# Optimization experiments

Hardware: AMD Instinct MI355X
Metric: run time of the kernel (lower is better)

Reference implementation:

```python
import jax, jax.numpy as jnp
import numpy as np

B, N, D, K = 16, 65536, 24, 512
ATTRACTION_WEIGHT = 1.0
REPULSION_WEIGHT = 1.5
MARGIN_WEIGHT = 5.0
THRESHOLD = 0.5
MARGIN = 0.2
TAU = 0.7


def setup_inputs() -> dict:
    key = jax.random.key(0)
    k1, k2, k3 = jax.random.split(key, 3)
    beta = jax.random.normal(k1, (B, N, 1), jnp.float32)
    embed = jax.random.normal(k2, (B, N, D), jnp.float32)
    # First K hits of each event are the condensation points (one per instance),
    # remaining hits get a random instance id in [0, K).
    rand_sid = jax.random.randint(k3, (B, N - K), 0, K, jnp.int32)
    cp_sid = jnp.broadcast_to(jnp.arange(K, dtype=jnp.int32), (B, K))
    slice_id = jnp.concatenate([cp_sid, rand_sid], axis=1)
    is_cp = jnp.concatenate(
        [jnp.ones((B, K), jnp.int32), jnp.zeros((B, N - K), jnp.int32)], axis=1)
    return {"beta": beta, "embed": embed, "slice_id": slice_id, "is_cp": is_cp}


def _per_batch(beta_b, emb_b, sid, cp):
    # beta_b: [N], emb_b: [N, D], sid: [N] int, cp: [N] int
    n = beta_b.shape[0]
    f32 = beta_b.dtype
    cp_mask = cp == 1
    pos_count = cp_mask.sum()
    neg_count = n - pos_count

    seg_cnt = jax.ops.segment_sum(jnp.ones((n,), f32), sid, num_segments=K)
    inst_present = seg_cnt > 0
    cp_per_inst = jax.ops.segment_sum(cp_mask.astype(f32), sid, num_segments=K)
    valid_inst = inst_present & (cp_per_inst == 1)  # inst_cp.sum() == 1

    # --- grouped softmax CE over each instance (temperature TAU) ---
    logits = jnp.clip(beta_b, -20.0, 20.0) / TAU
    seg_max = jax.ops.segment_max(logits, sid, num_segments=K)
    safe_max = jnp.where(inst_present, seg_max, 0.0)
    ex = jnp.exp(logits - safe_max[sid])
    denom = jax.ops.segment_sum(ex, sid, num_segments=K)
    cp_logit = jax.ops.segment_sum(jnp.where(cp_mask, logits, 0.0), sid,
                                   num_segments=K)  # exactly one cp when valid
    p_cp = jnp.exp(cp_logit - safe_max) / jnp.maximum(denom, 1e-30)
    loss_inst = -jnp.log(p_cp + 1e-9)
    slice_count = valid_inst.sum()
    beta_slice_ce = jnp.where(valid_inst, loss_inst, 0.0).sum() / jnp.maximum(slice_count, 1)

    # --- margin loss on sigmoid(beta) ---
    beta_prob = jax.nn.sigmoid(jnp.clip(beta_b, -20.0, 20.0))
    pos_m = jnp.where(cp_mask, jax.nn.relu(THRESHOLD + MARGIN - beta_prob), 0.0).sum() \
        / jnp.maximum(pos_count, 1)
    neg_m = jnp.where(cp_mask, 0.0, jax.nn.relu(beta_prob - (THRESHOLD - MARGIN))).sum() \
        / jnp.maximum(neg_count, 1)
    beta_loss = beta_slice_ce + MARGIN_WEIGHT * (pos_m + neg_m)

    # --- attraction: hits pulled to first CP of their instance ---
    idx = jnp.arange(n, dtype=jnp.int32)
    first_cp = jax.ops.segment_min(jnp.where(cp_mask, idx, n), sid, num_segments=K)
    has_cp = (first_cp < n) & inst_present
    cp_emb = emb_b[jnp.minimum(first_cp, n - 1)]  # [K, D]
    d2 = jnp.minimum(((emb_b - cp_emb[sid]) ** 2).sum(-1), 50.0)
    d2_mean = jax.ops.segment_sum(d2, sid, num_segments=K) / jnp.maximum(seg_cnt, 1.0)
    attraction = ATTRACTION_WEIGHT * jnp.where(has_cp, d2_mean, 0.0).sum()

    # --- repulsion: pairwise exp(-d2) between CP embeddings (incl. diagonal) ---
    m = has_cp.astype(f32)
    mcount = m.sum()
    sq = (cp_emb ** 2).sum(-1)
    pd2 = sq[:, None] + sq[None, :] - 2.0 * (cp_emb @ cp_emb.T)
    pd2 = jnp.clip(pd2, 0.0, 50.0)
    rep = (jnp.exp(-pd2) * (m[:, None] * m[None, :])).sum() / jnp.maximum(mcount * mcount, 1.0)
    repulsion = jnp.where(mcount > 1, REPULSION_WEIGHT * rep, 0.0)

    valid = (pos_count >= 1) & (neg_count >= 1) & (slice_count > 0)
    total = beta_loss + attraction + repulsion
    return total, beta_loss, attraction, repulsion, valid


def reference(beta, embed, slice_id, is_cp):
    beta = jnp.nan_to_num(jnp.squeeze(beta, -1), nan=0.0, posinf=0.0, neginf=0.0)
    embed = jnp.nan_to_num(embed, nan=0.0, posinf=0.0, neginf=0.0)
    total, bl, al, rl, valid = jax.vmap(_per_batch)(beta, embed, slice_id, is_cp)
    v = valid.astype(beta.dtype)
    count = v.sum()
    safe = jnp.maximum(count, 1.0)
    ok = count > 0
    final = jnp.where(ok, (total * v).sum() / safe, 0.0)
    beta_log = jnp.where(ok, (bl * v).sum() / safe, 0.0)
    attr_log = jnp.where(ok, (al * v).sum() / safe, 0.0)
    repl_log = jnp.where(ok, (rl * v).sum() / safe, 0.0)
    return final, beta_log, attr_log, repl_log
```

## Files before the change

kernel.cpp:

```cpp
#include <hip/hip_runtime.h>
#include <math.h>

#define BB 16
#define NN 65536
#define DD 24
#define KK 512
#define CH 64
#define HPB (NN / CH)
#define TPB 256
#define RPB 8

__device__ __forceinline__ float fixnum(float v) {
  return __builtin_isfinite(v) ? v : 0.0f;
}

__device__ __forceinline__ float blockReduceSum(float v, float* sbuf) {
  __syncthreads();
  #pragma unroll
  for (int off = 32; off > 0; off >>= 1) v += __shfl_down(v, off, 64);
  int wid = threadIdx.x >> 6, lane = threadIdx.x & 63;
  if (lane == 0) sbuf[wid] = v;
  __syncthreads();
  return sbuf[0] + sbuf[1] + sbuf[2] + sbuf[3];
}

__global__ __launch_bounds__(TPB) void k1_seg(
    const float* __restrict__ beta, const int* __restrict__ sid,
    const int* __restrict__ iscp,
    float* __restrict__ cnt_p, float* __restrict__ den_p,
    float* __restrict__ cpc_p, float* __restrict__ cpl_p,
    int* __restrict__ first_p, float* __restrict__ marg_p)
{
  __shared__ float s_cnt[KK], s_den[KK], s_cpc[KK], s_cpl[KK];
  __shared__ int   s_first[KK];
  __shared__ float sred[4];
  int b = blockIdx.x >> 6, c = blockIdx.x & 63, t = threadIdx.x;
  for (int k = t; k < KK; k += TPB) {
    s_cnt[k] = 0.f; s_den[k] = 0.f; s_cpc[k] = 0.f; s_cpl[k] = 0.f; s_first[k] = NN;
  }
  __syncthreads();
  int h0 = c * HPB + t * 4;
  size_t g0 = (size_t)b * NN + h0;
  float4 bv = *(const float4*)(beta + g0);
  int4   sv = *(const int4*)(sid + g0);
  int4   cv = *(const int4*)(iscp + g0);
  float pm = 0.f, nm = 0.f;
  float bs[4] = {bv.x, bv.y, bv.z, bv.w};
  int   ss[4] = {sv.x, sv.y, sv.z, sv.w};
  int   cs[4] = {cv.x, cv.y, cv.z, cv.w};
  #pragma unroll
  for (int j = 0; j < 4; ++j) {
    float bc = fminf(fmaxf(fixnum(bs[j]), -20.f), 20.f);
    float logit = bc * (1.0f / 0.7f);
    int s = ss[j];
    atomicAdd(&s_cnt[s], 1.0f);
    atomicAdd(&s_den[s], __expf(logit));
    float prob = 1.0f / (1.0f + __expf(-bc));
    if (cs[j] == 1) {
      atomicAdd(&s_cpc[s], 1.0f);
      atomicAdd(&s_cpl[s], logit);
      atomicMin(&s_first[s], h0 + j);
      pm += fmaxf(0.7f - prob, 0.f);
    } else {
      nm += fmaxf(prob - 0.3f, 0.f);
    }
  }
  float pms = blockReduceSum(pm, sred);
  float nms = blockReduceSum(nm, sred);
  if (t == 0) { marg_p[2 * blockIdx.x] = pms; marg_p[2 * blockIdx.x + 1] = nms; }
  __syncthreads();
  size_t base = ((size_t)b * CH + c) * KK;
  for (int k = t; k < KK; k += TPB) {
    cnt_p[base + k] = s_cnt[k]; den_p[base + k] = s_den[k];
    cpc_p[base + k] = s_cpc[k]; cpl_p[base + k] = s_cpl[k];
    first_p[base + k] = s_first[k];
  }
}

__global__ __launch_bounds__(TPB) void k2_fin(
    const float* __restrict__ embed,
    const float* __restrict__ cnt_p, const float* __restrict__ den_p,
    const float* __restrict__ cpc_p, const float* __restrict__ cpl_p,
    const int* __restrict__ first_p,
    float* __restrict__ seg_cnt, float* __restrict__ loss_v,
    float* __restrict__ valid_f, float* __restrict__ has_cp_f,
    float* __restrict__ cpc_tot, float* __restrict__ cp_emb,
    float* __restrict__ d2_acc, float* __restrict__ rep_acc)
{
  int idx = blockIdx.x * TPB + threadIdx.x;
  int b = idx >> 9, k = idx & (KK - 1);
  float cnt = 0.f, den = 0.f, cpc = 0.f, cpl = 0.f;
  int fc = NN;
  #pragma unroll 8
  for (int c = 0; c < CH; ++c) {
    size_t base = ((size_t)b * CH + c) * KK + k;
    cnt += cnt_p[base]; den += den_p[base];
    cpc += cpc_p[base]; cpl += cpl_p[base];
    fc = min(fc, first_p[base]);
  }
  bool present = cnt > 0.f;
  bool vinst = present && (cpc == 1.0f);
  float p = __expf(cpl) / fmaxf(den, 1e-30f);
  seg_cnt[idx] = cnt;
  cpc_tot[idx] = cpc;
  loss_v[idx] = vinst ? -__logf(p + 1e-9f) : 0.f;
  valid_f[idx] = vinst ? 1.f : 0.f;
  has_cp_f[idx] = ((fc < NN) && present) ? 1.f : 0.f;
  d2_acc[idx] = 0.f;
  if (idx < BB) rep_acc[idx] = 0.f;
  int row = fc < NN ? fc : NN - 1;
  const float4* src = (const float4*)(embed + ((size_t)b * NN + row) * DD);
  float4* dst = (float4*)(cp_emb + (size_t)idx * DD);
  #pragma unroll
  for (int q = 0; q < DD / 4; ++q) {
    float4 v = src[q];
    v.x = fixnum(v.x); v.y = fixnum(v.y); v.z = fixnum(v.z); v.w = fixnum(v.w);
    dst[q] = v;
  }
}

__global__ __launch_bounds__(TPB) void k3_attr_rep(
    const float* __restrict__ embed, const int* __restrict__ sid,
    const float* __restrict__ cp_emb, const float* __restrict__ has_cp_f,
    float* __restrict__ d2_acc, float* __restrict__ rep_acc)
{
  __shared__ float s_d2[KK];
  __shared__ float sred[4];
  int b = blockIdx.x >> 6, c = blockIdx.x & 63, t = threadIdx.x;
  for (int k = t; k < KK; k += TPB) s_d2[k] = 0.f;
  __syncthreads();
  const float* cebase = cp_emb + (size_t)b * KK * DD;
  #pragma unroll
  for (int i = 0; i < HPB / TPB; ++i) {
    int h = c * HPB + i * TPB + t;
    size_t g = (size_t)b * NN + h;
    int s = sid[g];
    const float4* e  = (const float4*)(embed + g * DD);
    const float4* ce = (const float4*)(cebase + (size_t)s * DD);
    float d2 = 0.f;
    #pragma unroll
    for (int q = 0; q < DD / 4; ++q) {
      float4 ev = e[q]; float4 cv = ce[q];
      float x;
      x = fixnum(ev.x) - cv.x; d2 += x * x;
      x = fixnum(ev.y) - cv.y; d2 += x * x;
      x = fixnum(ev.z) - cv.z; d2 += x * x;
      x = fixnum(ev.w) - cv.w; d2 += x * x;
    }
    atomicAdd(&s_d2[s], fminf(d2, 50.f));
  }
  __syncthreads();
  for (int k = t; k < KK; k += TPB)
    atomicAdd(&d2_acc[b * KK + k], s_d2[k]);

  int j0 = t, j1 = t + TPB;
  float cj0[DD], cj1[DD];
  const float4* cj0p = (const float4*)(cebase + (size_t)j0 * DD);
  const float4* cj1p = (const float4*)(cebase + (size_t)j1 * DD);
  #pragma unroll
  for (int q = 0; q < DD / 4; ++q) {
    float4 a = cj0p[q], bq = cj1p[q];
    cj0[q*4] = a.x; cj0[q*4+1] = a.y; cj0[q*4+2] = a.z; cj0[q*4+3] = a.w;
    cj1[q*4] = bq.x; cj1[q*4+1] = bq.y; cj1[q*4+2] = bq.z; cj1[q*4+3] = bq.w;
  }
  float m0 = has_cp_f[b * KK + j0], m1 = has_cp_f[b * KK + j1];
  float acc = 0.f;
  #pragma unroll
  for (int ri = 0; ri < RPB; ++ri) {
    int i = c * RPB + ri;
    float mi = has_cp_f[b * KK + i];
    float d20 = 0.f, d21 = 0.f;
    #pragma unroll
    for (int d = 0; d < DD; ++d) {
      float ci = cebase[i * DD + d];
      float x0 = ci - cj0[d]; d20 += x0 * x0;
      float x1 = ci - cj1[d]; d21 += x1 * x1;
    }
    acc += mi * (m0 * __expf(-fminf(d20, 50.f)) + m1 * __expf(-fminf(d21, 50.f)));
  }
  float tot = blockReduceSum(acc, sred);
  if (t == 0) atomicAdd(&rep_acc[b], tot);
}

__global__ __launch_bounds__(1024) void k4_final(
    const float* __restrict__ d2_acc, const float* __restrict__ seg_cnt,
    const float* __restrict__ loss_v, const float* __restrict__ valid_f,
    const float* __restrict__ cpc_tot, const float* __restrict__ has_cp_f,
    const float* __restrict__ marg_p, const float* __restrict__ rep_acc,
    float* __restrict__ out)
{
  __shared__ float s_b[BB][5];
  int w = threadIdx.x >> 6, l = threadIdx.x & 63;
  int b = w;
  float attr = 0.f, ce = 0.f, vcnt = 0.f, pcnt = 0.f, mcnt = 0.f;
  #pragma unroll
  for (int k = l; k < KK; k += 64) {
    int idx = b * KK + k;
    float hc = has_cp_f[idx];
    attr += hc * (d2_acc[idx] / fmaxf(seg_cnt[idx], 1.f));
    ce   += loss_v[idx];
    vcnt += valid_f[idx];
    pcnt += cpc_tot[idx];
    mcnt += hc;
  }
  float pm = marg_p[(b * CH + l) * 2];
  float nm = marg_p[(b * CH + l) * 2 + 1];
  #pragma unroll
  for (int off = 32; off > 0; off >>= 1) {
    attr += __shfl_down(attr, off, 64);
    ce   += __shfl_down(ce, off, 64);
    vcnt += __shfl_down(vcnt, off, 64);
    pcnt += __shfl_down(pcnt, off, 64);
    mcnt += __shfl_down(mcnt, off, 64);
    pm   += __shfl_down(pm, off, 64);
    nm   += __shfl_down(nm, off, 64);
  }
  if (l == 0) {
    float pos = pcnt, neg = (float)NN - pos;
    float slice_ce = ce / fmaxf(vcnt, 1.f);
    float beta_loss = slice_ce + 5.0f * (pm / fmaxf(pos, 1.f) + nm / fmaxf(neg, 1.f));
    float rep = rep_acc[b] / fmaxf(mcnt * mcnt, 1.f);
    float repulsion = (mcnt > 1.f) ? 1.5f * rep : 0.f;
    float v = (pos >= 1.f && neg >= 1.f && vcnt > 0.f) ? 1.f : 0.f;
    s_b[w][0] = (beta_loss + attr + repulsion) * v;
    s_b[w][1] = beta_loss * v;
    s_b[w][2] = attr * v;
    s_b[w][3] = repulsion * v;
    s_b[w][4] = v;
  }
  __syncthreads();
  if (threadIdx.x == 0) {
    float s0 = 0.f, s1 = 0.f, s2 = 0.f, s3 = 0.f, cv = 0.f;
    #pragma unroll
    for (int i = 0; i < BB; ++i) {
      s0 += s_b[i][0]; s1 += s_b[i][1]; s2 += s_b[i][2]; s3 += s_b[i][3]; cv += s_b[i][4];
    }
    float safe = fmaxf(cv, 1.f);
    bool ok = cv > 0.f;
    out[0] = ok ? s0 / safe : 0.f;
    out[1] = ok ? s1 / safe : 0.f;
    out[2] = ok ? s2 / safe : 0.f;
    out[3] = ok ? s3 / safe : 0.f;
  }
}

extern "C" void kernel_launch(void* const* d_in, const int* in_sizes, int n_in,
                              void* d_out, int out_size, void* d_ws, size_t ws_size,
                              hipStream_t stream) {
  (void)in_sizes; (void)n_in; (void)out_size; (void)ws_size;
  const float* beta  = (const float*)d_in[0];
  const float* embed = (const float*)d_in[1];
  const int*   sid   = (const int*)d_in[2];
  const int*   iscp  = (const int*)d_in[3];
  float* out = (float*)d_out;
  char* ws = (char*)d_ws;

  size_t off = 0;
  auto alloc = [&](size_t bytes) {
    size_t o = off; off += (bytes + 255) & ~(size_t)255; return o;
  };
  const size_t BCK = (size_t)BB * CH * KK * 4;
  const size_t BKf = (size_t)BB * KK * 4;
  size_t o_cnt_p  = alloc(BCK);
  size_t o_den_p  = alloc(BCK);
  size_t o_cpc_p  = alloc(BCK);
  size_t o_cpl_p  = alloc(BCK);
  size_t o_first  = alloc(BCK);
  size_t o_marg   = alloc((size_t)BB * CH * 2 * 4);
  size_t o_segc   = alloc(BKf);
  size_t o_lossv  = alloc(BKf);
  size_t o_validf = alloc(BKf);
  size_t o_hascp  = alloc(BKf);
  size_t o_cpct   = alloc(BKf);
  size_t o_d2     = alloc(BKf);
  size_t o_cpe    = alloc((size_t)BB * KK * DD * 4);
  size_t o_rep    = alloc((size_t)BB * 4);

  k1_seg<<<BB * CH, TPB, 0, stream>>>(beta, sid, iscp,
      (float*)(ws + o_cnt_p), (float*)(ws + o_den_p),
      (float*)(ws + o_cpc_p), (float*)(ws + o_cpl_p),
      (int*)(ws + o_first), (float*)(ws + o_marg));

  k2_fin<<<(BB * KK) / TPB, TPB, 0, stream>>>(embed,
      (const float*)(ws + o_cnt_p), (const float*)(ws + o_den_p),
      (const float*)(ws + o_cpc_p), (const float*)(ws + o_cpl_p),
      (const int*)(ws + o_first),
      (float*)(ws + o_segc), (float*)(ws + o_lossv), (float*)(ws + o_validf),
      (float*)(ws + o_hascp), (float*)(ws + o_cpct), (float*)(ws + o_cpe),
      (float*)(ws + o_d2), (float*)(ws + o_rep));

  k3_attr_rep<<<BB * CH, TPB, 0, stream>>>(embed, sid,
      (const float*)(ws + o_cpe), (const float*)(ws + o_hascp),
      (float*)(ws + o_d2), (float*)(ws + o_rep));

  k4_final<<<1, 1024, 0, stream>>>((const float*)(ws + o_d2),
      (const float*)(ws + o_segc), (const float*)(ws + o_lossv),
      (const float*)(ws + o_validf), (const float*)(ws + o_cpct),
      (const float*)(ws + o_hascp), (const float*)(ws + o_marg),
      (const float*)(ws + o_rep), out);
}
```

Before: 200.3 us.

## Fuse four kernels into one cooperative kernel with grid syncs

Replaces the four-kernel pipeline with a single cooperative kernel that runs the segment pass, the finalisation, the attraction/repulsion pass and the final reduction as phases separated by grid.sync(). The chunk count per event is halved to 32, so the grid is 512 blocks (each k1-phase thread handles 8 hits and each block does 16 repulsion rows), and the finalisation phase uses 16-lane shuffle reductions. The aim is to remove kernel launch gaps and tail effects, at the cost of grid-wide barriers, reduced parallelism in the embed-heavy phase, and the requirement that all blocks be co-resident.

```diff
diff --git a/kernel.cpp b/kernel.cpp
--- a/kernel.cpp
+++ b/kernel.cpp
@@ -1,14 +1,17 @@
 #include <hip/hip_runtime.h>
+#include <hip/hip_cooperative_groups.h>
 #include <math.h>
+
+namespace cg = cooperative_groups;
 
 #define BB 16
 #define NN 65536
 #define DD 24
 #define KK 512
-#define CH 64
+#define CH 32
 #define HPB (NN / CH)
 #define TPB 256
-#define RPB 8
+#define RPB 16
 
 __device__ __forceinline__ float fixnum(float v) {
   return __builtin_isfinite(v) ? v : 0.0f;
@@ -24,223 +27,229 @@
   return sbuf[0] + sbuf[1] + sbuf[2] + sbuf[3];
 }
 
-__global__ __launch_bounds__(TPB) void k1_seg(
+__global__ __launch_bounds__(TPB, 2) void fused_all(
     const float* __restrict__ beta, const int* __restrict__ sid,
-    const int* __restrict__ iscp,
+    const int* __restrict__ iscp, const float* __restrict__ embed,
     float* __restrict__ cnt_p, float* __restrict__ den_p,
     float* __restrict__ cpc_p, float* __restrict__ cpl_p,
-    int* __restrict__ first_p, float* __restrict__ marg_p)
-{
-  __shared__ float s_cnt[KK], s_den[KK], s_cpc[KK], s_cpl[KK];
-  __shared__ int   s_first[KK];
-  __shared__ float sred[4];
-  int b = blockIdx.x >> 6, c = blockIdx.x & 63, t = threadIdx.x;
-  for (int k = t; k < KK; k += TPB) {
-    s_cnt[k] = 0.f; s_den[k] = 0.f; s_cpc[k] = 0.f; s_cpl[k] = 0.f; s_first[k] = NN;
-  }
-  __syncthreads();
-  int h0 = c * HPB + t * 4;
-  size_t g0 = (size_t)b * NN + h0;
-  float4 bv = *(const float4*)(beta + g0);
-  int4   sv = *(const int4*)(sid + g0);
-  int4   cv = *(const int4*)(iscp + g0);
-  float pm = 0.f, nm = 0.f;
-  float bs[4] = {bv.x, bv.y, bv.z, bv.w};
-  int   ss[4] = {sv.x, sv.y, sv.z, sv.w};
-  int   cs[4] = {cv.x, cv.y, cv.z, cv.w};
-  #pragma unroll
-  for (int j = 0; j < 4; ++j) {
-    float bc = fminf(fmaxf(fixnum(bs[j]), -20.f), 20.f);
-    float logit = bc * (1.0f / 0.7f);
-    int s = ss[j];
-    atomicAdd(&s_cnt[s], 1.0f);
-    atomicAdd(&s_den[s], __expf(logit));
-    float prob = 1.0f / (1.0f + __expf(-bc));
-    if (cs[j] == 1) {
-      atomicAdd(&s_cpc[s], 1.0f);
-      atomicAdd(&s_cpl[s], logit);
-      atomicMin(&s_first[s], h0 + j);
-      pm += fmaxf(0.7f - prob, 0.f);
-    } else {
-      nm += fmaxf(prob - 0.3f, 0.f);
-    }
-  }
-  float pms = blockReduceSum(pm, sred);
-  float nms = blockReduceSum(nm, sred);
-  if (t == 0) { marg_p[2 * blockIdx.x] = pms; marg_p[2 * blockIdx.x + 1] = nms; }
-  __syncthreads();
-  size_t base = ((size_t)b * CH + c) * KK;
-  for (int k = t; k < KK; k += TPB) {
-    cnt_p[base + k] = s_cnt[k]; den_p[base + k] = s_den[k];
-    cpc_p[base + k] = s_cpc[k]; cpl_p[base + k] = s_cpl[k];
-    first_p[base + k] = s_first[k];
-  }
-}
-
-__global__ __launch_bounds__(TPB) void k2_fin(
-    const float* __restrict__ embed,
-    const float* __restrict__ cnt_p, const float* __restrict__ den_p,
-    const float* __restrict__ cpc_p, const float* __restrict__ cpl_p,
-    const int* __restrict__ first_p,
+    int* __restrict__ first_p, float* __restrict__ marg_p,
     float* __restrict__ seg_cnt, float* __restrict__ loss_v,
     float* __restrict__ valid_f, float* __restrict__ has_cp_f,
     float* __restrict__ cpc_tot, float* __restrict__ cp_emb,
-    float* __restrict__ d2_acc, float* __restrict__ rep_acc)
+    float* __restrict__ d2_acc, float* __restrict__ rep_acc,
+    float* __restrict__ out)
 {
-  int idx = blockIdx.x * TPB + threadIdx.x;
-  int b = idx >> 9, k = idx & (KK - 1);
-  float cnt = 0.f, den = 0.f, cpc = 0.f, cpl = 0.f;
-  int fc = NN;
-  #pragma unroll 8
-  for (int c = 0; c < CH; ++c) {
-    size_t base = ((size_t)b * CH + c) * KK + k;
-    cnt += cnt_p[base]; den += den_p[base];
-    cpc += cpc_p[base]; cpl += cpl_p[base];
-    fc = min(fc, first_p[base]);
-  }
-  bool present = cnt > 0.f;
-  bool vinst = present && (cpc == 1.0f);
-  float p = __expf(cpl) / fmaxf(den, 1e-30f);
-  seg_cnt[idx] = cnt;
-  cpc_tot[idx] = cpc;
-  loss_v[idx] = vinst ? -__logf(p + 1e-9f) : 0.f;
-  valid_f[idx] = vinst ? 1.f : 0.f;
-  has_cp_f[idx] = ((fc < NN) && present) ? 1.f : 0.f;
-  d2_acc[idx] = 0.f;
-  if (idx < BB) rep_acc[idx] = 0.f;
-  int row = fc < NN ? fc : NN - 1;
-  const float4* src = (const float4*)(embed + ((size_t)b * NN + row) * DD);
-  float4* dst = (float4*)(cp_emb + (size_t)idx * DD);
-  #pragma unroll
-  for (int q = 0; q < DD / 4; ++q) {
-    float4 v = src[q];
-    v.x = fixnum(v.x); v.y = fixnum(v.y); v.z = fixnum(v.z); v.w = fixnum(v.w);
-    dst[q] = v;
-  }
-}
-
-__global__ __launch_bounds__(TPB) void k3_attr_rep(
-    const float* __restrict__ embed, const int* __restrict__ sid,
-    const float* __restrict__ cp_emb, const float* __restrict__ has_cp_f,
-    float* __restrict__ d2_acc, float* __restrict__ rep_acc)
-{
+  cg::grid_group grid = cg::this_grid();
+  __shared__ float s_cnt[KK], s_den[KK], s_cpc[KK], s_cpl[KK];
+  __shared__ int   s_first[KK];
   __shared__ float s_d2[KK];
   __shared__ float sred[4];
-  int b = blockIdx.x >> 6, c = blockIdx.x & 63, t = threadIdx.x;
-  for (int k = t; k < KK; k += TPB) s_d2[k] = 0.f;
+  __shared__ float s_b[BB][5];
+
+  int b = blockIdx.x / CH, c = blockIdx.x % CH, t = threadIdx.x;
+
+  for (int k = t; k < KK; k += TPB) {
+    s_cnt[k] = 0.f; s_den[k] = 0.f; s_cpc[k] = 0.f; s_cpl[k] = 0.f; s_first[k] = NN;
+  }
   __syncthreads();
-  const float* cebase = cp_emb + (size_t)b * KK * DD;
-  #pragma unroll
-  for (int i = 0; i < HPB / TPB; ++i) {
-    int h = c * HPB + i * TPB + t;
-    size_t g = (size_t)b * NN + h;
-    int s = sid[g];
-    const float4* e  = (const float4*)(embed + g * DD);
-    const float4* ce = (const float4*)(cebase + (size_t)s * DD);
-    float d2 = 0.f;
+  {
+    int h0 = c * HPB + t * 8;
+    size_t g0 = (size_t)b * NN + h0;
+    float pm = 0.f, nm = 0.f;
+    #pragma unroll
+    for (int half = 0; half < 2; ++half) {
+      size_t g = g0 + half * 4;
+      float4 bv = *(const float4*)(beta + g);
+      int4   sv = *(const int4*)(sid + g);
+      int4   cv = *(const int4*)(iscp + g);
+      float bs[4] = {bv.x, bv.y, bv.z, bv.w};
+      int   ss[4] = {sv.x, sv.y, sv.z, sv.w};
+      int   cs[4] = {cv.x, cv.y, cv.z, cv.w};
+      #pragma unroll
+      for (int j = 0; j < 4; ++j) {
+        float bc = fminf(fmaxf(fixnum(bs[j]), -20.f), 20.f);
+        float logit = bc * (1.0f / 0.7f);
+        int s = ss[j];
+        atomicAdd(&s_cnt[s], 1.0f);
+        atomicAdd(&s_den[s], __expf(logit));
+        float prob = 1.0f / (1.0f + __expf(-bc));
+        if (cs[j] == 1) {
+          atomicAdd(&s_cpc[s], 1.0f);
+          atomicAdd(&s_cpl[s], logit);
+          atomicMin(&s_first[s], h0 + half * 4 + j);
+          pm += fmaxf(0.7f - prob, 0.f);
+        } else {
+          nm += fmaxf(prob - 0.3f, 0.f);
+        }
+      }
+    }
+    float pms = blockReduceSum(pm, sred);
+    float nms = blockReduceSum(nm, sred);
+    if (t == 0) { marg_p[2 * blockIdx.x] = pms; marg_p[2 * blockIdx.x + 1] = nms; }
+    __syncthreads();
+    size_t base = ((size_t)b * CH + c) * KK;
+    for (int k = t; k < KK; k += TPB) {
+      cnt_p[base + k] = s_cnt[k]; den_p[base + k] = s_den[k];
+      cpc_p[base + k] = s_cpc[k]; cpl_p[base + k] = s_cpl[k];
+      first_p[base + k] = s_first[k];
+    }
+  }
+  grid.sync();
+
+  {
+    int sub = t >> 4, lane16 = t & 15;
+    int idx = blockIdx.x * 16 + sub;
+    int pb = idx >> 9, pk = idx & (KK - 1);
+    size_t base0 = ((size_t)pb * CH + lane16) * KK + pk;
+    size_t base1 = ((size_t)pb * CH + lane16 + 16) * KK + pk;
+    float cnt = cnt_p[base0] + cnt_p[base1];
+    float den = den_p[base0] + den_p[base1];
+    float cpc = cpc_p[base0] + cpc_p[base1];
+    float cpl = cpl_p[base0] + cpl_p[base1];
+    int fc = min(first_p[base0], first_p[base1]);
+    #pragma unroll
+    for (int m = 8; m > 0; m >>= 1) {
+      cnt += __shfl_xor(cnt, m, 16);
+      den += __shfl_xor(den, m, 16);
+      cpc += __shfl_xor(cpc, m, 16);
+      cpl += __shfl_xor(cpl, m, 16);
+      fc = min(fc, __shfl_xor(fc, m, 16));
+    }
+    if (lane16 == 0) {
+      bool present = cnt > 0.f;
+      bool vinst = present && (cpc == 1.0f);
+      float p = __expf(cpl) / fmaxf(den, 1e-30f);
+      seg_cnt[idx] = cnt;
+      cpc_tot[idx] = cpc;
+      loss_v[idx] = vinst ? -__logf(p + 1e-9f) : 0.f;
+      valid_f[idx] = vinst ? 1.f : 0.f;
+      has_cp_f[idx] = ((fc < NN) && present) ? 1.f : 0.f;
+      d2_acc[idx] = 0.f;
+      if (idx < BB) rep_acc[idx] = 0.f;
+    }
+    int row = fc < NN ? fc : NN - 1;
+    if (lane16 < DD / 4) {
+      const float4* src = (const float4*)(embed + ((size_t)pb * NN + row) * DD);
+      float4 v = src[lane16];
+      v.x = fixnum(v.x); v.y = fixnum(v.y); v.z = fixnum(v.z); v.w = fixnum(v.w);
+      ((float4*)(cp_emb + (size_t)idx * DD))[lane16] = v;
+    }
+  }
+  grid.sync();
+
+  {
+    for (int k = t; k < KK; k += TPB) s_d2[k] = 0.f;
+    __syncthreads();
+    const float* cebase = cp_emb + (size_t)b * KK * DD;
+    #pragma unroll
+    for (int i = 0; i < HPB / TPB; ++i) {
+      int h = c * HPB + i * TPB + t;
+      size_t g = (size_t)b * NN + h;
+      int s = sid[g];
+      const float4* e  = (const float4*)(embed + g * DD);
+      const float4* ce = (const float4*)(cebase + (size_t)s * DD);
+      float d2 = 0.f;
+      #pragma unroll
+      for (int q = 0; q < DD / 4; ++q) {
+        float4 ev = e[q]; float4 cv = ce[q];
+        float x;
+        x = fixnum(ev.x) - cv.x; d2 += x * x;
+        x = fixnum(ev.y) - cv.y; d2 += x * x;
+        x = fixnum(ev.z) - cv.z; d2 += x * x;
+        x = fixnum(ev.w) - cv.w; d2 += x * x;
+      }
+      atomicAdd(&s_d2[s], fminf(d2, 50.f));
+    }
+    __syncthreads();
+    for (int k = t; k < KK; k += TPB)
+      atomicAdd(&d2_acc[b * KK + k], s_d2[k]);
+
+    int j0 = t, j1 = t + TPB;
+    float cj0[DD], cj1[DD];
+    const float4* cj0p = (const float4*)(cebase + (size_t)j0 * DD);
+    const float4* cj1p = (const float4*)(cebase + (size_t)j1 * DD);
     #pragma unroll
     for (int q = 0; q < DD / 4; ++q) {
-      float4 ev = e[q]; float4 cv = ce[q];
-      float x;
-      x = fixnum(ev.x) - cv.x; d2 += x * x;
-      x = fixnum(ev.y) - cv.y; d2 += x * x;
-      x = fixnum(ev.z) - cv.z; d2 += x * x;
-      x = fixnum(ev.w) - cv.w; d2 += x * x;
-    }
-    atomicAdd(&s_d2[s], fminf(d2, 50.f));
-  }
-  __syncthreads();
-  for (int k = t; k < KK; k += TPB)
-    atomicAdd(&d2_acc[b * KK + k], s_d2[k]);
-
-  int j0 = t, j1 = t + TPB;
-  float cj0[DD], cj1[DD];
-  const float4* cj0p = (const float4*)(cebase + (size_t)j0 * DD);
-  const float4* cj1p = (const float4*)(cebase + (size_t)j1 * DD);
-  #pragma unroll
-  for (int q = 0; q < DD / 4; ++q) {
-    float4 a = cj0p[q], bq = cj1p[q];
-    cj0[q*4] = a.x; cj0[q*4+1] = a.y; cj0[q*4+2] = a.z; cj0[q*4+3] = a.w;
-    cj1[q*4] = bq.x; cj1[q*4+1] = bq.y; cj1[q*4+2] = bq.z; cj1[q*4+3] = bq.w;
-  }
-  float m0 = has_cp_f[b * KK + j0], m1 = has_cp_f[b * KK + j1];
-  float acc = 0.f;
-  #pragma unroll
-  for (int ri = 0; ri < RPB; ++ri) {
-    int i = c * RPB + ri;
-    float mi = has_cp_f[b * KK + i];
-    float d20 = 0.f, d21 = 0.f;
-    #pragma unroll
-    for (int d = 0; d < DD; ++d) {
-      float ci = cebase[i * DD + d];
-      float x0 = ci - cj0[d]; d20 += x0 * x0;
-      float x1 = ci - cj1[d]; d21 += x1 * x1;
-    }
-    acc += mi * (m0 * __expf(-fminf(d20, 50.f)) + m1 * __expf(-fminf(d21, 50.f)));
-  }
-  float tot = blockReduceSum(acc, sred);
-  if (t == 0) atomicAdd(&rep_acc[b], tot);
-}
-
-__global__ __launch_bounds__(1024) void k4_final(
-    const float* __restrict__ d2_acc, const float* __restrict__ seg_cnt,
-    const float* __restrict__ loss_v, const float* __restrict__ valid_f,
-    const float* __restrict__ cpc_tot, const float* __restrict__ has_cp_f,
-    const float* __restrict__ marg_p, const float* __restrict__ rep_acc,
-    float* __restrict__ out)
-{
-  __shared__ float s_b[BB][5];
-  int w = threadIdx.x >> 6, l = threadIdx.x & 63;
-  int b = w;
-  float attr = 0.f, ce = 0.f, vcnt = 0.f, pcnt = 0.f, mcnt = 0.f;
-  #pragma unroll
-  for (int k = l; k < KK; k += 64) {
-    int idx = b * KK + k;
-    float hc = has_cp_f[idx];
-    attr += hc * (d2_acc[idx] / fmaxf(seg_cnt[idx], 1.f));
-    ce   += loss_v[idx];
-    vcnt += valid_f[idx];
-    pcnt += cpc_tot[idx];
-    mcnt += hc;
-  }
-  float pm = marg_p[(b * CH + l) * 2];
-  float nm = marg_p[(b * CH + l) * 2 + 1];
-  #pragma unroll
-  for (int off = 32; off > 0; off >>= 1) {
-    attr += __shfl_down(attr, off, 64);
-    ce   += __shfl_down(ce, off, 64);
-    vcnt += __shfl_down(vcnt, off, 64);
-    pcnt += __shfl_down(pcnt, off, 64);
-    mcnt += __shfl_down(mcnt, off, 64);
-    pm   += __shfl_down(pm, off, 64);
-    nm   += __shfl_down(nm, off, 64);
-  }
-  if (l == 0) {
-    float pos = pcnt, neg = (float)NN - pos;
-    float slice_ce = ce / fmaxf(vcnt, 1.f);
-    float beta_loss = slice_ce + 5.0f * (pm / fmaxf(pos, 1.f) + nm / fmaxf(neg, 1.f));
-    float rep = rep_acc[b] / fmaxf(mcnt * mcnt, 1.f);
-    float repulsion = (mcnt > 1.f) ? 1.5f * rep : 0.f;
-    float v = (pos >= 1.f && neg >= 1.f && vcnt > 0.f) ? 1.f : 0.f;
-    s_b[w][0] = (beta_loss + attr + repulsion) * v;
-    s_b[w][1] = beta_loss * v;
-    s_b[w][2] = attr * v;
-    s_b[w][3] = repulsion * v;
-    s_b[w][4] = v;
-  }
-  __syncthreads();
-  if (threadIdx.x == 0) {
-    float s0 = 0.f, s1 = 0.f, s2 = 0.f, s3 = 0.f, cv = 0.f;
-    #pragma unroll
-    for (int i = 0; i < BB; ++i) {
-      s0 += s_b[i][0]; s1 += s_b[i][1]; s2 += s_b[i][2]; s3 += s_b[i][3]; cv += s_b[i][4];
-    }
-    float safe = fmaxf(cv, 1.f);
-    bool ok = cv > 0.f;
-    out[0] = ok ? s0 / safe : 0.f;
-    out[1] = ok ? s1 / safe : 0.f;
-    out[2] = ok ? s2 / safe : 0.f;
-    out[3] = ok ? s3 / safe : 0.f;
+      float4 a = cj0p[q], bq = cj1p[q];
+      cj0[q*4] = a.x; cj0[q*4+1] = a.y; cj0[q*4+2] = a.z; cj0[q*4+3] = a.w;
+      cj1[q*4] = bq.x; cj1[q*4+1] = bq.y; cj1[q*4+2] = bq.z; cj1[q*4+3] = bq.w;
+    }
+    float m0 = has_cp_f[b * KK + j0], m1 = has_cp_f[b * KK + j1];
+    float acc = 0.f;
+    #pragma unroll
+    for (int ri = 0; ri < RPB; ++ri) {
+      int i = c * RPB + ri;
+      float mi = has_cp_f[b * KK + i];
+      float d20 = 0.f, d21 = 0.f;
+      #pragma unroll
+      for (int d = 0; d < DD; ++d) {
+        float ci = cebase[i * DD + d];
+        float x0 = ci - cj0[d]; d20 += x0 * x0;
+        float x1 = ci - cj1[d]; d21 += x1 * x1;
+      }
+      acc += mi * (m0 * __expf(-fminf(d20, 50.f)) + m1 * __expf(-fminf(d21, 50.f)));
+    }
+    float tot = blockReduceSum(acc, sred);
+    if (t == 0) atomicAdd(&rep_acc[b], tot);
+  }
+  grid.sync();
+
+  if (blockIdx.x == 0) {
+    int w = t >> 6, l = t & 63;
+    #pragma unroll
+    for (int bb = 0; bb < 4; ++bb) {
+      int fb = w * 4 + bb;
+      float attr = 0.f, ce = 0.f, vcnt = 0.f, pcnt = 0.f, mcnt = 0.f;
+      #pragma unroll
+      for (int k = l; k < KK; k += 64) {
+        int idx = fb * KK + k;
+        float hc = has_cp_f[idx];
+        attr += hc * (d2_acc[idx] / fmaxf(seg_cnt[idx], 1.f));
+        ce   += loss_v[idx];
+        vcnt += valid_f[idx];
+        pcnt += cpc_tot[idx];
+        mcnt += hc;
+      }
+      float pm = (l < CH) ? marg_p[(fb * CH + l) * 2]     : 0.f;
+      float nm = (l < CH) ? marg_p[(fb * CH + l) * 2 + 1] : 0.f;
+      #pragma unroll
+      for (int off = 32; off > 0; off >>= 1) {
+        attr += __shfl_down(attr, off, 64);
+        ce   += __shfl_down(ce, off, 64);
+        vcnt += __shfl_down(vcnt, off, 64);
+        pcnt += __shfl_down(pcnt, off, 64);
+        mcnt += __shfl_down(mcnt, off, 64);
+        pm   += __shfl_down(pm, off, 64);
+        nm   += __shfl_down(nm, off, 64);
+      }
+      if (l == 0) {
+        float pos = pcnt, neg = (float)NN - pos;
+        float slice_ce = ce / fmaxf(vcnt, 1.f);
+        float beta_loss = slice_ce + 5.0f * (pm / fmaxf(pos, 1.f) + nm / fmaxf(neg, 1.f));
+        float rep = rep_acc[fb] / fmaxf(mcnt * mcnt, 1.f);
+        float repulsion = (mcnt > 1.f) ? 1.5f * rep : 0.f;
+        float v = (pos >= 1.f && neg >= 1.f && vcnt > 0.f) ? 1.f : 0.f;
+        s_b[fb][0] = (beta_loss + attr + repulsion) * v;
+        s_b[fb][1] = beta_loss * v;
+        s_b[fb][2] = attr * v;
+        s_b[fb][3] = repulsion * v;
+        s_b[fb][4] = v;
+      }
+    }
+    __syncthreads();
+    if (t == 0) {
+      float s0 = 0.f, s1 = 0.f, s2 = 0.f, s3 = 0.f, cv = 0.f;
+      #pragma unroll
+      for (int i = 0; i < BB; ++i) {
+        s0 += s_b[i][0]; s1 += s_b[i][1]; s2 += s_b[i][2]; s3 += s_b[i][3]; cv += s_b[i][4];
+      }
+      float safe = fmaxf(cv, 1.f);
+      bool ok = cv > 0.f;
+      out[0] = ok ? s0 / safe : 0.f;
+      out[1] = ok ? s1 / safe : 0.f;
+      out[2] = ok ? s2 / safe : 0.f;
+      out[3] = ok ? s3 / safe : 0.f;
+    }
   }
 }
 
@@ -276,26 +285,29 @@
   size_t o_cpe    = alloc((size_t)BB * KK * DD * 4);
   size_t o_rep    = alloc((size_t)BB * 4);
 
-  k1_seg<<<BB * CH, TPB, 0, stream>>>(beta, sid, iscp,
-      (float*)(ws + o_cnt_p), (float*)(ws + o_den_p),
-      (float*)(ws + o_cpc_p), (float*)(ws + o_cpl_p),
-      (int*)(ws + o_first), (float*)(ws + o_marg));
-
-  k2_fin<<<(BB * KK) / TPB, TPB, 0, stream>>>(embed,
-      (const float*)(ws + o_cnt_p), (const float*)(ws + o_den_p),
-      (const float*)(ws + o_cpc_p), (const float*)(ws + o_cpl_p),
-      (const int*)(ws + o_first),
-      (float*)(ws + o_segc), (float*)(ws + o_lossv), (float*)(ws + o_validf),
-      (float*)(ws + o_hascp), (float*)(ws + o_cpct), (float*)(ws + o_cpe),
-      (float*)(ws + o_d2), (float*)(ws + o_rep));
-
-  k3_attr_rep<<<BB * CH, TPB, 0, stream>>>(embed, sid,
-      (const float*)(ws + o_cpe), (const float*)(ws + o_hascp),
-      (float*)(ws + o_d2), (float*)(ws + o_rep));
-
-  k4_final<<<1, 1024, 0, stream>>>((const float*)(ws + o_d2),
-      (const float*)(ws + o_segc), (const float*)(ws + o_lossv),
-      (const float*)(ws + o_validf), (const float*)(ws + o_cpct),
-      (const float*)(ws + o_hascp), (const float*)(ws + o_marg),
-      (const float*)(ws + o_rep), out);
+  float* p_cnt  = (float*)(ws + o_cnt_p);
+  float* p_den  = (float*)(ws + o_den_p);
+  float* p_cpc  = (float*)(ws + o_cpc_p);
+  float* p_cpl  = (float*)(ws + o_cpl_p);
+  int*   p_fst  = (int*)(ws + o_first);
+  float* p_marg = (float*)(ws + o_marg);
+  float* p_segc = (float*)(ws + o_segc);
+  float* p_lv   = (float*)(ws + o_lossv);
+  float* p_vf   = (float*)(ws + o_validf);
+  float* p_hc   = (float*)(ws + o_hascp);
+  float* p_cpt  = (float*)(ws + o_cpct);
+  float* p_cpe  = (float*)(ws + o_cpe);
+  float* p_d2   = (float*)(ws + o_d2);
+  float* p_rep  = (float*)(ws + o_rep);
+
+  void* args[] = {
+    (void*)&beta, (void*)&sid, (void*)&iscp, (void*)&embed,
+    (void*)&p_cnt, (void*)&p_den, (void*)&p_cpc, (void*)&p_cpl,
+    (void*)&p_fst, (void*)&p_marg,
+    (void*)&p_segc, (void*)&p_lv, (void*)&p_vf, (void*)&p_hc,
+    (void*)&p_cpt, (void*)&p_cpe, (void*)&p_d2, (void*)&p_rep,
+    (void*)&out,
+  };
+  hipLaunchCooperativeKernel((const void*)fused_all, dim3(BB * CH), dim3(TPB),
+                             args, 0, stream);
 }
```

New measurement: 348.6 us. 74.0% more time.

## Fuse final reduction into attraction/repulsion kernel and halve k1 chunk count

Applied to the files above, without the earlier changes.

Folds the single-block final reduction into the attraction/repulsion kernel: the last block, found with an atomic done-counter and thread fences, reads the accumulators and writes the outputs, which removes one kernel launch. The segment-stats kernel now processes 8 hits per thread with 32 chunks per batch, halving the partial buffers that the finalize kernel must sum. The attraction loop is restructured to use a vectorized int4 sid load with 4 consecutive hits per thread. The cost is a serial tail where one block reduces all 16 batches, plus fewer blocks in k1 to fill the GPU.

```diff
diff --git a/kernel.cpp b/kernel.cpp
--- a/kernel.cpp
+++ b/kernel.cpp
@@ -5,8 +5,10 @@
 #define NN 65536
 #define DD 24
 #define KK 512
-#define CH 64
-#define HPB (NN / CH)
+#define CH1 32
+#define HPB1 (NN / CH1)
+#define CH3 64
+#define HPB3 (NN / CH3)
 #define TPB 256
 #define RPB 8
 
@@ -34,42 +36,46 @@
   __shared__ float s_cnt[KK], s_den[KK], s_cpc[KK], s_cpl[KK];
   __shared__ int   s_first[KK];
   __shared__ float sred[4];
-  int b = blockIdx.x >> 6, c = blockIdx.x & 63, t = threadIdx.x;
+  int b = blockIdx.x / CH1, c = blockIdx.x % CH1, t = threadIdx.x;
   for (int k = t; k < KK; k += TPB) {
     s_cnt[k] = 0.f; s_den[k] = 0.f; s_cpc[k] = 0.f; s_cpl[k] = 0.f; s_first[k] = NN;
   }
   __syncthreads();
-  int h0 = c * HPB + t * 4;
+  int h0 = c * HPB1 + t * 8;
   size_t g0 = (size_t)b * NN + h0;
-  float4 bv = *(const float4*)(beta + g0);
-  int4   sv = *(const int4*)(sid + g0);
-  int4   cv = *(const int4*)(iscp + g0);
   float pm = 0.f, nm = 0.f;
-  float bs[4] = {bv.x, bv.y, bv.z, bv.w};
-  int   ss[4] = {sv.x, sv.y, sv.z, sv.w};
-  int   cs[4] = {cv.x, cv.y, cv.z, cv.w};
   #pragma unroll
-  for (int j = 0; j < 4; ++j) {
-    float bc = fminf(fmaxf(fixnum(bs[j]), -20.f), 20.f);
-    float logit = bc * (1.0f / 0.7f);
-    int s = ss[j];
-    atomicAdd(&s_cnt[s], 1.0f);
-    atomicAdd(&s_den[s], __expf(logit));
-    float prob = 1.0f / (1.0f + __expf(-bc));
-    if (cs[j] == 1) {
-      atomicAdd(&s_cpc[s], 1.0f);
-      atomicAdd(&s_cpl[s], logit);
-      atomicMin(&s_first[s], h0 + j);
-      pm += fmaxf(0.7f - prob, 0.f);
-    } else {
-      nm += fmaxf(prob - 0.3f, 0.f);
+  for (int half = 0; half < 2; ++half) {
+    size_t g = g0 + half * 4;
+    float4 bv = *(const float4*)(beta + g);
+    int4   sv = *(const int4*)(sid + g);
+    int4   cv = *(const int4*)(iscp + g);
+    float bs[4] = {bv.x, bv.y, bv.z, bv.w};
+    int   ss[4] = {sv.x, sv.y, sv.z, sv.w};
+    int   cs[4] = {cv.x, cv.y, cv.z, cv.w};
+    #pragma unroll
+    for (int j = 0; j < 4; ++j) {
+      float bc = fminf(fmaxf(fixnum(bs[j]), -20.f), 20.f);
+      float logit = bc * (1.0f / 0.7f);
+      int s = ss[j];
+      atomicAdd(&s_cnt[s], 1.0f);
+      atomicAdd(&s_den[s], __expf(logit));
+      float prob = 1.0f / (1.0f + __expf(-bc));
+      if (cs[j] == 1) {
+        atomicAdd(&s_cpc[s], 1.0f);
+        atomicAdd(&s_cpl[s], logit);
+        atomicMin(&s_first[s], h0 + half * 4 + j);
+        pm += fmaxf(0.7f - prob, 0.f);
+      } else {
+        nm += fmaxf(prob - 0.3f, 0.f);
+      }
     }
   }
   float pms = blockReduceSum(pm, sred);
   float nms = blockReduceSum(nm, sred);
   if (t == 0) { marg_p[2 * blockIdx.x] = pms; marg_p[2 * blockIdx.x + 1] = nms; }
   __syncthreads();
-  size_t base = ((size_t)b * CH + c) * KK;
+  size_t base = ((size_t)b * CH1 + c) * KK;
   for (int k = t; k < KK; k += TPB) {
     cnt_p[base + k] = s_cnt[k]; den_p[base + k] = s_den[k];
     cpc_p[base + k] = s_cpc[k]; cpl_p[base + k] = s_cpl[k];
@@ -85,15 +91,16 @@
     float* __restrict__ seg_cnt, float* __restrict__ loss_v,
     float* __restrict__ valid_f, float* __restrict__ has_cp_f,
     float* __restrict__ cpc_tot, float* __restrict__ cp_emb,
-    float* __restrict__ d2_acc, float* __restrict__ rep_acc)
+    float* __restrict__ d2_acc, float* __restrict__ rep_acc,
+    unsigned* __restrict__ done)
 {
   int idx = blockIdx.x * TPB + threadIdx.x;
   int b = idx >> 9, k = idx & (KK - 1);
   float cnt = 0.f, den = 0.f, cpc = 0.f, cpl = 0.f;
   int fc = NN;
   #pragma unroll 8
-  for (int c = 0; c < CH; ++c) {
-    size_t base = ((size_t)b * CH + c) * KK + k;
+  for (int c = 0; c < CH1; ++c) {
+    size_t base = ((size_t)b * CH1 + c) * KK + k;
     cnt += cnt_p[base]; den += den_p[base];
     cpc += cpc_p[base]; cpl += cpl_p[base];
     fc = min(fc, first_p[base]);
@@ -108,6 +115,7 @@
   has_cp_f[idx] = ((fc < NN) && present) ? 1.f : 0.f;
   d2_acc[idx] = 0.f;
   if (idx < BB) rep_acc[idx] = 0.f;
+  if (idx == 0) *done = 0u;
   int row = fc < NN ? fc : NN - 1;
   const float4* src = (const float4*)(embed + ((size_t)b * NN + row) * DD);
   float4* dst = (float4*)(cp_emb + (size_t)idx * DD);
@@ -119,128 +127,147 @@
   }
 }
 
-__global__ __launch_bounds__(TPB) void k3_attr_rep(
+__global__ __launch_bounds__(TPB) void k3_attr_rep_fin(
     const float* __restrict__ embed, const int* __restrict__ sid,
     const float* __restrict__ cp_emb, const float* __restrict__ has_cp_f,
-    float* __restrict__ d2_acc, float* __restrict__ rep_acc)
+    const float* __restrict__ seg_cnt, const float* __restrict__ loss_v,
+    const float* __restrict__ valid_f, const float* __restrict__ cpc_tot,
+    const float* __restrict__ marg_p,
+    float* __restrict__ d2_acc, float* __restrict__ rep_acc,
+    unsigned* __restrict__ done, float* __restrict__ out)
 {
   __shared__ float s_d2[KK];
   __shared__ float sred[4];
-  int b = blockIdx.x >> 6, c = blockIdx.x & 63, t = threadIdx.x;
+  __shared__ float s_b[BB][5];
+  __shared__ int amLast;
+  int b = blockIdx.x / CH3, c = blockIdx.x % CH3, t = threadIdx.x;
   for (int k = t; k < KK; k += TPB) s_d2[k] = 0.f;
   __syncthreads();
   const float* cebase = cp_emb + (size_t)b * KK * DD;
-  #pragma unroll
-  for (int i = 0; i < HPB / TPB; ++i) {
-    int h = c * HPB + i * TPB + t;
-    size_t g = (size_t)b * NN + h;
-    int s = sid[g];
-    const float4* e  = (const float4*)(embed + g * DD);
-    const float4* ce = (const float4*)(cebase + (size_t)s * DD);
-    float d2 = 0.f;
-    #pragma unroll
-    for (int q = 0; q < DD / 4; ++q) {
-      float4 ev = e[q]; float4 cv = ce[q];
-      float x;
-      x = fixnum(ev.x) - cv.x; d2 += x * x;
-      x = fixnum(ev.y) - cv.y; d2 += x * x;
-      x = fixnum(ev.z) - cv.z; d2 += x * x;
-      x = fixnum(ev.w) - cv.w; d2 += x * x;
-    }
-    atomicAdd(&s_d2[s], fminf(d2, 50.f));
+  {
+    int h0 = c * HPB3 + t * 4;
+    size_t g0 = (size_t)b * NN + h0;
+    int4 sv = *(const int4*)(sid + g0);
+    int ss[4] = {sv.x, sv.y, sv.z, sv.w};
+    #pragma unroll
+    for (int j = 0; j < 4; ++j) {
+      const float4* e  = (const float4*)(embed + (g0 + j) * DD);
+      const float4* ce = (const float4*)(cebase + (size_t)ss[j] * DD);
+      float d2 = 0.f;
+      #pragma unroll
+      for (int q = 0; q < DD / 4; ++q) {
+        float4 ev = e[q]; float4 cv = ce[q];
+        float x;
+        x = fixnum(ev.x) - cv.x; d2 += x * x;
+        x = fixnum(ev.y) - cv.y; d2 += x * x;
+        x = fixnum(ev.z) - cv.z; d2 += x * x;
+        x = fixnum(ev.w) - cv.w; d2 += x * x;
+      }
+      atomicAdd(&s_d2[ss[j]], fminf(d2, 50.f));
+    }
   }
   __syncthreads();
   for (int k = t; k < KK; k += TPB)
     atomicAdd(&d2_acc[b * KK + k], s_d2[k]);
 
-  int j0 = t, j1 = t + TPB;
-  float cj0[DD], cj1[DD];
-  const float4* cj0p = (const float4*)(cebase + (size_t)j0 * DD);
-  const float4* cj1p = (const float4*)(cebase + (size_t)j1 * DD);
-  #pragma unroll
-  for (int q = 0; q < DD / 4; ++q) {
-    float4 a = cj0p[q], bq = cj1p[q];
-    cj0[q*4] = a.x; cj0[q*4+1] = a.y; cj0[q*4+2] = a.z; cj0[q*4+3] = a.w;
-    cj1[q*4] = bq.x; cj1[q*4+1] = bq.y; cj1[q*4+2] = bq.z; cj1[q*4+3] = bq.w;
-  }
-  float m0 = has_cp_f[b * KK + j0], m1 = has_cp_f[b * KK + j1];
-  float acc = 0.f;
-  #pragma unroll
-  for (int ri = 0; ri < RPB; ++ri) {
-    int i = c * RPB + ri;
-    float mi = has_cp_f[b * KK + i];
-    float d20 = 0.f, d21 = 0.f;
-    #pragma unroll
-    for (int d = 0; d < DD; ++d) {
-      float ci = cebase[i * DD + d];
-      float x0 = ci - cj0[d]; d20 += x0 * x0;
-      float x1 = ci - cj1[d]; d21 += x1 * x1;
-    }
-    acc += mi * (m0 * __expf(-fminf(d20, 50.f)) + m1 * __expf(-fminf(d21, 50.f)));
-  }
-  float tot = blockReduceSum(acc, sred);
-  if (t == 0) atomicAdd(&rep_acc[b], tot);
-}
-
-__global__ __launch_bounds__(1024) void k4_final(
-    const float* __restrict__ d2_acc, const float* __restrict__ seg_cnt,
-    const float* __restrict__ loss_v, const float* __restrict__ valid_f,
-    const float* __restrict__ cpc_tot, const float* __restrict__ has_cp_f,
-    const float* __restrict__ marg_p, const float* __restrict__ rep_acc,
-    float* __restrict__ out)
-{
-  __shared__ float s_b[BB][5];
-  int w = threadIdx.x >> 6, l = threadIdx.x & 63;
-  int b = w;
-  float attr = 0.f, ce = 0.f, vcnt = 0.f, pcnt = 0.f, mcnt = 0.f;
-  #pragma unroll
-  for (int k = l; k < KK; k += 64) {
-    int idx = b * KK + k;
-    float hc = has_cp_f[idx];
-    attr += hc * (d2_acc[idx] / fmaxf(seg_cnt[idx], 1.f));
-    ce   += loss_v[idx];
-    vcnt += valid_f[idx];
-    pcnt += cpc_tot[idx];
-    mcnt += hc;
-  }
-  float pm = marg_p[(b * CH + l) * 2];
-  float nm = marg_p[(b * CH + l) * 2 + 1];
-  #pragma unroll
-  for (int off = 32; off > 0; off >>= 1) {
-    attr += __shfl_down(attr, off, 64);
-    ce   += __shfl_down(ce, off, 64);
-    vcnt += __shfl_down(vcnt, off, 64);
-    pcnt += __shfl_down(pcnt, off, 64);
-    mcnt += __shfl_down(mcnt, off, 64);
-    pm   += __shfl_down(pm, off, 64);
-    nm   += __shfl_down(nm, off, 64);
-  }
-  if (l == 0) {
-    float pos = pcnt, neg = (float)NN - pos;
-    float slice_ce = ce / fmaxf(vcnt, 1.f);
-    float beta_loss = slice_ce + 5.0f * (pm / fmaxf(pos, 1.f) + nm / fmaxf(neg, 1.f));
-    float rep = rep_acc[b] / fmaxf(mcnt * mcnt, 1.f);
-    float repulsion = (mcnt > 1.f) ? 1.5f * rep : 0.f;
-    float v = (pos >= 1.f && neg >= 1.f && vcnt > 0.f) ? 1.f : 0.f;
-    s_b[w][0] = (beta_loss + attr + repulsion) * v;
-    s_b[w][1] = beta_loss * v;
-    s_b[w][2] = attr * v;
-    s_b[w][3] = repulsion * v;
-    s_b[w][4] = v;
-  }
-  __syncthreads();
-  if (threadIdx.x == 0) {
-    float s0 = 0.f, s1 = 0.f, s2 = 0.f, s3 = 0.f, cv = 0.f;
-    #pragma unroll
-    for (int i = 0; i < BB; ++i) {
-      s0 += s_b[i][0]; s1 += s_b[i][1]; s2 += s_b[i][2]; s3 += s_b[i][3]; cv += s_b[i][4];
-    }
-    float safe = fmaxf(cv, 1.f);
-    bool ok = cv > 0.f;
-    out[0] = ok ? s0 / safe : 0.f;
-    out[1] = ok ? s1 / safe : 0.f;
-    out[2] = ok ? s2 / safe : 0.f;
-    out[3] = ok ? s3 / safe : 0.f;
+  {
+    int j0 = t, j1 = t + TPB;
+    float cj0[DD], cj1[DD];
+    const float4* cj0p = (const float4*)(cebase + (size_t)j0 * DD);
+    const float4* cj1p = (const float4*)(cebase + (size_t)j1 * DD);
+    #pragma unroll
+    for (int q = 0; q < DD / 4; ++q) {
+      float4 a = cj0p[q], bq = cj1p[q];
+      cj0[q*4] = a.x; cj0[q*4+1] = a.y; cj0[q*4+2] = a.z; cj0[q*4+3] = a.w;
+      cj1[q*4] = bq.x; cj1[q*4+1] = bq.y; cj1[q*4+2] = bq.z; cj1[q*4+3] = bq.w;
+    }
+    float m0 = has_cp_f[b * KK + j0], m1 = has_cp_f[b * KK + j1];
+    float acc = 0.f;
+    #pragma unroll
+    for (int ri = 0; ri < RPB; ++ri) {
+      int i = c * RPB + ri;
+      float mi = has_cp_f[b * KK + i];
+      float d20 = 0.f, d21 = 0.f;
+      #pragma unroll
+      for (int d = 0; d < DD; ++d) {
+        float ci = cebase[i * DD + d];
+        float x0 = ci - cj0[d]; d20 += x0 * x0;
+        float x1 = ci - cj1[d]; d21 += x1 * x1;
+      }
+      acc += mi * (m0 * __expf(-fminf(d20, 50.f)) + m1 * __expf(-fminf(d21, 50.f)));
+    }
+    float tot = blockReduceSum(acc, sred);
+    if (t == 0) atomicAdd(&rep_acc[b], tot);
+  }
+
+  __syncthreads();
+  if (t == 0) {
+    __threadfence();
+    unsigned old = atomicAdd(done, 1u);
+    amLast = (old == (unsigned)(BB * CH3 - 1));
+  }
+  __syncthreads();
+  if (amLast) {
+    __threadfence();
+    int w = t >> 6, l = t & 63;
+    #pragma unroll
+    for (int bb = 0; bb < 4; ++bb) {
+      int fb = w * 4 + bb;
+      float attr = 0.f, ce = 0.f, vcnt = 0.f, pcnt = 0.f, mcnt = 0.f;
+      #pragma unroll
+      for (int k = l; k < KK; k += 64) {
+        int idx = fb * KK + k;
+        float hc = has_cp_f[idx];
+        float dv = __hip_atomic_load(&d2_acc[idx], __ATOMIC_RELAXED,
+                                     __HIP_MEMORY_SCOPE_AGENT);
+        attr += hc * (dv / fmaxf(seg_cnt[idx], 1.f));
+        ce   += loss_v[idx];
+        vcnt += valid_f[idx];
+        pcnt += cpc_tot[idx];
+        mcnt += hc;
+      }
+      float pm = (l < CH1) ? marg_p[(fb * CH1 + l) * 2]     : 0.f;
+      float nm = (l < CH1) ? marg_p[(fb * CH1 + l) * 2 + 1] : 0.f;
+      #pragma unroll
+      for (int off = 32; off > 0; off >>= 1) {
+        attr += __shfl_down(attr, off, 64);
+        ce   += __shfl_down(ce, off, 64);
+        vcnt += __shfl_down(vcnt, off, 64);
+        pcnt += __shfl_down(pcnt, off, 64);
+        mcnt += __shfl_down(mcnt, off, 64);
+        pm   += __shfl_down(pm, off, 64);
+        nm   += __shfl_down(nm, off, 64);
+      }
+      if (l == 0) {
+        float pos = pcnt, neg = (float)NN - pos;
+        float slice_ce = ce / fmaxf(vcnt, 1.f);
+        float beta_loss = slice_ce + 5.0f * (pm / fmaxf(pos, 1.f) + nm / fmaxf(neg, 1.f));
+        float repv = __hip_atomic_load(&rep_acc[fb], __ATOMIC_RELAXED,
+                                       __HIP_MEMORY_SCOPE_AGENT);
+        float rep = repv / fmaxf(mcnt * mcnt, 1.f);
+        float repulsion = (mcnt > 1.f) ? 1.5f * rep : 0.f;
+        float v = (pos >= 1.f && neg >= 1.f && vcnt > 0.f) ? 1.f : 0.f;
+        s_b[fb][0] = (beta_loss + attr + repulsion) * v;
+        s_b[fb][1] = beta_loss * v;
+        s_b[fb][2] = attr * v;
+        s_b[fb][3] = repulsion * v;
+        s_b[fb][4] = v;
+      }
+    }
+    __syncthreads();
+    if (t == 0) {
+      float s0 = 0.f, s1 = 0.f, s2 = 0.f, s3 = 0.f, cv = 0.f;
+      #pragma unroll
+      for (int i = 0; i < BB; ++i) {
+        s0 += s_b[i][0]; s1 += s_b[i][1]; s2 += s_b[i][2]; s3 += s_b[i][3]; cv += s_b[i][4];
+      }
+      float safe = fmaxf(cv, 1.f);
+      bool ok = cv > 0.f;
+      out[0] = ok ? s0 / safe : 0.f;
+      out[1] = ok ? s1 / safe : 0.f;
+      out[2] = ok ? s2 / safe : 0.f;
+      out[3] = ok ? s3 / safe : 0.f;
+    }
   }
 }
 
@@ -259,14 +286,14 @@
   auto alloc = [&](size_t bytes) {
     size_t o = off; off += (bytes + 255) & ~(size_t)255; return o;
   };
-  const size_t BCK = (size_t)BB * CH * KK * 4;
+  const size_t BCK = (size_t)BB * CH1 * KK * 4;
   const size_t BKf = (size_t)BB * KK * 4;
   size_t o_cnt_p  = alloc(BCK);
   size_t o_den_p  = alloc(BCK);
   size_t o_cpc_p  = alloc(BCK);
   size_t o_cpl_p  = alloc(BCK);
   size_t o_first  = alloc(BCK);
-  size_t o_marg   = alloc((size_t)BB * CH * 2 * 4);
+  size_t o_marg   = alloc((size_t)BB * CH1 * 2 * 4);
   size_t o_segc   = alloc(BKf);
   size_t o_lossv  = alloc(BKf);
   size_t o_validf = alloc(BKf);
@@ -275,8 +302,9 @@
   size_t o_d2     = alloc(BKf);
   size_t o_cpe    = alloc((size_t)BB * KK * DD * 4);
   size_t o_rep    = alloc((size_t)BB * 4);
-
-  k1_seg<<<BB * CH, TPB, 0, stream>>>(beta, sid, iscp,
+  size_t o_done   = alloc(256);
+
+  k1_seg<<<BB * CH1, TPB, 0, stream>>>(beta, sid, iscp,
       (float*)(ws + o_cnt_p), (float*)(ws + o_den_p),
       (float*)(ws + o_cpc_p), (float*)(ws + o_cpl_p),
       (int*)(ws + o_first), (float*)(ws + o_marg));
@@ -287,15 +315,13 @@
       (const int*)(ws + o_first),
       (float*)(ws + o_segc), (float*)(ws + o_lossv), (float*)(ws + o_validf),
       (float*)(ws + o_hascp), (float*)(ws + o_cpct), (float*)(ws + o_cpe),
-      (float*)(ws + o_d2), (float*)(ws + o_rep));
-
-  k3_attr_rep<<<BB * CH, TPB, 0, stream>>>(embed, sid,
+      (float*)(ws + o_d2), (float*)(ws + o_rep), (unsigned*)(ws + o_done));
+
+  k3_attr_rep_fin<<<BB * CH3, TPB, 0, stream>>>(embed, sid,
       (const float*)(ws + o_cpe), (const float*)(ws + o_hascp),
-      (float*)(ws + o_d2), (float*)(ws + o_rep));
-
-  k4_final<<<1, 1024, 0, stream>>>((const float*)(ws + o_d2),
       (const float*)(ws + o_segc), (const float*)(ws + o_lossv),
       (const float*)(ws + o_validf), (const float*)(ws + o_cpct),
-      (const float*)(ws + o_hascp), (const float*)(ws + o_marg),
-      (const float*)(ws + o_rep), out);
-}
+      (const float*)(ws + o_marg),
+      (float*)(ws + o_d2), (float*)(ws + o_rep),
+      (unsigned*)(ws + o_done), out);
+}
```

Measured after the change: 241.6 us. 1.21x slower.
